# Kernel tuning notes

Measured on AMD Instinct MI355X. Metric: run time of the kernel, lower is better.

The kernel has to match this reference:

```python
import jax, jax.numpy as jnp
import numpy as np

N = 4096        # number_of_users
IN = 1000       # in_size (items)
H1, H2 = 2048, 1024
EMB = 512
HEADS = 8
OUT = 1000


def setup_inputs() -> dict:
    key = jax.random.key(0)
    ks = iter(jax.random.split(key, 32))
    def lin(i, o):
        return jax.random.normal(next(ks), (i, o), jnp.float32) * (1.0 / np.sqrt(i))
    inp = {"batch": jax.random.normal(next(ks), (N, IN), jnp.float32)}
    for p in ("q", "k", "v"):
        inp[p + "_w1"] = lin(IN, H1); inp[p + "_b1"] = jnp.zeros((H1,), jnp.float32)
        inp[p + "_w2"] = lin(H1, H2); inp[p + "_b2"] = jnp.zeros((H2,), jnp.float32)
        inp[p + "_w3"] = lin(H2, EMB); inp[p + "_b3"] = jnp.zeros((EMB,), jnp.float32)
    inp["wo_w"] = lin(EMB, OUT)
    inp["wo_b"] = jnp.zeros((OUT,), jnp.float32)
    return inp


def _mlp(x, w1, b1, w2, b2, w3, b3):
    h = jax.nn.relu(x @ w1 + b1)
    h = jax.nn.relu(h @ w2 + b2)
    return h @ w3 + b3


def _split_heads(x):
    # [N, EMB] -> [HEADS, N, depth]
    return x.reshape(N, HEADS, EMB // HEADS).transpose(1, 0, 2)


def reference(batch,
              q_w1, q_b1, q_w2, q_b2, q_w3, q_b3,
              k_w1, k_b1, k_w2, k_b2, k_w3, k_b3,
              v_w1, v_b1, v_w2, v_b2, v_w3, v_b3,
              wo_w, wo_b):
    q = _mlp(batch, q_w1, q_b1, q_w2, q_b2, q_w3, q_b3)
    k = _mlp(batch, k_w1, k_b1, k_w2, k_b2, k_w3, k_b3)
    v = _mlp(batch, v_w1, v_b1, v_w2, v_b2, v_w3, v_b3)
    qh = jax.nn.relu(_split_heads(q))
    kh = jax.nn.relu(_split_heads(k))
    vh = _split_heads(v)
    depth = EMB // HEADS
    # ReLU-normalized attention (no softmax): scores / row-sum
    scores = jnp.einsum('hnd,hmd->hnm', qh, kh) / jnp.sqrt(jnp.float32(depth))
    denom = jnp.sum(scores, axis=-1, keepdims=True) + 1e-8
    weights = scores / denom
    att = jnp.einsum('hnm,hmd->hnd', weights, vh)   # [H, N, depth]
    att = att.transpose(1, 0, 2).reshape(N, EMB)
    return att @ wo_w + wo_b
```

## Files before the change

kernel.cpp:

```cpp
#include <hip/hip_runtime.h>
#include <hip/hip_bf16.h>


typedef __attribute__((ext_vector_type(4))) float f32x4;
typedef __attribute__((ext_vector_type(4))) float float4v;
typedef __attribute__((ext_vector_type(8))) short bf16x8;

static constexpr size_t OFF_XB   = 0;
static constexpr size_t OFF_WT1  = OFF_XB   + 8388608;
static constexpr size_t OFF_WT2  = OFF_WT1  + 12582912;
static constexpr size_t OFF_WT3  = OFF_WT2  + 12582912;
static constexpr size_t OFF_MWT  = OFF_WT3  + 3145728;
static constexpr size_t OFF_B1C  = OFF_MWT  + 1048576;
static constexpr size_t OFF_H1   = OFF_B1C  + 24576;
static constexpr size_t OFF_H2   = OFF_H1   + 50331648;
static constexpr size_t OFF_QKV  = OFF_H2   + 25165824;
static constexpr size_t OFF_MP   = OFF_QKV  + 12582912;
static constexpr size_t OFF_MF   = OFF_MP   + 4259840;
static constexpr size_t OFF_QT   = OFF_MF   + 133120;

__device__ __forceinline__ void gload16(const __hip_bfloat16* g, __hip_bfloat16* l) {
  __builtin_amdgcn_global_load_lds(
      (const __attribute__((address_space(1))) void*)g,
      (__attribute__((address_space(3))) void*)l, 16, 0, 0);
}

__device__ __forceinline__ void xcd_map(int gx, int gy, int cm, int cn,
                                        int& zz, int& mt, int& nt) {
  const int gid = (blockIdx.z * gy + blockIdx.y) * gx + blockIdx.x;
  const int xcd = gid & 7;
  const int slot = gid >> 3;
  const int per = cm * cn;
  zz = slot / per;
  const int rem = slot % per;
  const int nxr = gx / cn;
  const int xr = xcd % nxr, yr = xcd / nxr;
  mt = yr * cm + rem % cm;
  nt = xr * cn + rem / cm;
}

__global__ __launch_bounds__(256) void prep(
    const float* __restrict__ w1a, const float* __restrict__ w1b, const float* __restrict__ w1c,
    const float* __restrict__ w2a, const float* __restrict__ w2b, const float* __restrict__ w2c,
    const float* __restrict__ w3a, const float* __restrict__ w3b, const float* __restrict__ w3c,
    const float* __restrict__ batch,
    __hip_bfloat16* __restrict__ WT1, __hip_bfloat16* __restrict__ WT2,
    __hip_bfloat16* __restrict__ WT3, __hip_bfloat16* __restrict__ XB) {
  const int b = blockIdx.x, t = threadIdx.x;
  if (b >= 3456) {
    int idx = (b - 3456) * 256 + t;
    int row = idx >> 8, c4 = (idx & 255) * 4;
    __hip_bfloat16 o[4];
    if (c4 < 1000) {
      float4v v = *reinterpret_cast<const float4v*>(&batch[(size_t)row * 1000 + c4]);
#pragma unroll
      for (int j = 0; j < 4; ++j) o[j] = __float2bfloat16(v[j]);
    } else {
#pragma unroll
      for (int j = 0; j < 4; ++j) o[j] = __float2bfloat16(0.f);
    }
    *reinterpret_cast<ushort4*>(&XB[(size_t)row * 1024 + c4]) =
        *reinterpret_cast<const ushort4*>(o);
    return;
  }
  __shared__ float tl[64][65];
  const float* in; __hip_bfloat16* out; int K, N, Kpad, kb, nb;
  if (b < 1536) {
    int mat = b / 512, r = b % 512;
    const float* s[3] = {w1a, w1b, w1c};
    in = s[mat]; out = WT1 + (size_t)mat * 2048 * 1024;
    K = 1000; N = 2048; Kpad = 1024; kb = r & 15; nb = r >> 4;
  } else if (b < 3072) {
    int r = b - 1536; int mat = r / 512; r %= 512;
    const float* s[3] = {w2a, w2b, w2c};
    in = s[mat]; out = WT2 + (size_t)mat * 1024 * 2048;
    K = 2048; N = 1024; Kpad = 2048; kb = r & 31; nb = r >> 5;
  } else {
    int r = b - 3072; int mat = r / 128; r %= 128;
    const float* s[3] = {w3a, w3b, w3c};
    in = s[mat]; out = WT3 + (size_t)mat * 512 * 1024;
    K = 1024; N = 512; Kpad = 1024; kb = r & 15; nb = r >> 4;
  }
  const int kb64 = kb * 64, nb64 = nb * 64;
  const int trow = t >> 4, tc4 = (t & 15) * 4;
#pragma unroll
  for (int it = 0; it < 4; ++it) {
    const int kl = it * 16 + trow;
    const int k = kb64 + kl;
    float4v v = {0.f, 0.f, 0.f, 0.f};
    if (k < K) v = *reinterpret_cast<const float4v*>(&in[(size_t)k * N + nb64 + tc4]);
    tl[kl][tc4 + 0] = v[0]; tl[kl][tc4 + 1] = v[1];
    tl[kl][tc4 + 2] = v[2]; tl[kl][tc4 + 3] = v[3];
  }
  __syncthreads();
  const int ln = t >> 2, ks = (t & 3) * 16;
  short ob[16];
#pragma unroll
  for (int u = 0; u < 16; ++u) {
    __hip_bfloat16 bb = __float2bfloat16(tl[ks + u][ln]);
    ob[u] = *(const short*)&bb;
  }
  __hip_bfloat16* dst = out + (size_t)(nb64 + ln) * Kpad + kb64 + ks;
  *reinterpret_cast<bf16x8*>(dst) = *reinterpret_cast<const bf16x8*>(&ob[0]);
  *reinterpret_cast<bf16x8*>(dst + 8) = *reinterpret_cast<const bf16x8*>(&ob[8]);
}

template <int NJ, int MINW>
__global__ __launch_bounds__(256, MINW) void gemm_fast(
    const __hip_bfloat16* __restrict__ A, int lda, size_t Az,
    const __hip_bfloat16* __restrict__ B, int ldb, size_t Bz,
    const float* __restrict__ bias0, const float* __restrict__ bias1,
    const float* __restrict__ bias2,
    void* __restrict__ Cout, int ldc, size_t Cz,
    int nlimit, int NT, int epi, int cm, int cn) {
  __shared__ __hip_bfloat16 smA[2][4096];
  __shared__ __hip_bfloat16 smB[2][NJ * 1024];
  const int t = threadIdx.x;
  int zz, mt, nt;
  xcd_map(gridDim.x, gridDim.y, cm, cn, zz, mt, nt);
  const int m0 = mt * 128, n0 = nt * (NJ * 32);
  A += (size_t)zz * Az;
  B += (size_t)zz * Bz;

  const int w = t >> 6, l = t & 63;
  const int wm = (w >> 1) * 64, wn = (w & 1) * (NJ * 16);
  const int fr = l & 15, fq = l >> 4;

  const int r0 = t >> 2;
  const int cg = (t & 3) ^ ((t >> 3) & 3);
  const __hip_bfloat16* gA0 = A + (size_t)(m0 + r0) * lda + cg * 8;
  const __hip_bfloat16* gA1 = gA0 + (size_t)64 * lda;
  const __hip_bfloat16* gB0 = B + (size_t)(n0 + r0) * ldb + cg * 8;
  const __hip_bfloat16* gB1 = gB0 + (size_t)64 * ldb;

  const int soff = (fq ^ ((fr >> 1) & 3)) * 8;
  int offA[4], offB[NJ];
#pragma unroll
  for (int i = 0; i < 4; ++i) offA[i] = (wm + i * 16 + fr) * 32 + soff;
#pragma unroll
  for (int j = 0; j < NJ; ++j) offB[j] = (wn + j * 16 + fr) * 32 + soff;

  f32x4 acc[4][NJ] = {};

  gload16(gA0, &smA[0][w * 512]);
  gload16(gA1, &smA[0][w * 512 + 2048]);
  gload16(gB0, &smB[0][w * 512]);
  if (NJ == 4) gload16(gB1, &smB[0][w * 512 + 2048]);

  for (int T = 0; T < NT; ++T) {
    const int cur = T & 1, nxt = cur ^ 1;
    __syncthreads();
    if (T + 1 < NT) {
      const size_t ko = (size_t)(T + 1) * 32;
      gload16(gA0 + ko, &smA[nxt][w * 512]);
      gload16(gA1 + ko, &smA[nxt][w * 512 + 2048]);
      gload16(gB0 + ko, &smB[nxt][w * 512]);
      if (NJ == 4) gload16(gB1 + ko, &smB[nxt][w * 512 + 2048]);
    }
    bf16x8 af[4], bf[NJ];
#pragma unroll
    for (int i = 0; i < 4; ++i)
      af[i] = *reinterpret_cast<const bf16x8*>(&smA[cur][offA[i]]);
#pragma unroll
    for (int j = 0; j < NJ; ++j)
      bf[j] = *reinterpret_cast<const bf16x8*>(&smB[cur][offB[j]]);
#pragma unroll
    for (int i = 0; i < 4; ++i)
#pragma unroll
      for (int j = 0; j < NJ; ++j)
        acc[i][j] = __builtin_amdgcn_mfma_f32_16x16x32_bf16(af[i], bf[j], acc[i][j], 0, 0, 0);
  }

  const float* bz = (zz == 0) ? bias0 : ((zz == 1) ? bias1 : bias2);
  const bool dorelu = (epi == 1) || (epi == 4) || (epi == 3 && zz < 2);
  float bv[NJ];
#pragma unroll
  for (int j = 0; j < NJ; ++j) {
    const int col = n0 + wn + j * 16 + fr;
    if (epi == 4) {
      const float* bsel = (col < 2048) ? bias0 : ((col < 4096) ? bias1 : bias2);
      bv[j] = bsel[col & 2047];
    } else if (epi == 2) {
      bv[j] = (col < nlimit) ? bias0[col] : 0.f;
    } else {
      bv[j] = bz[col];
    }
  }
#pragma unroll
  for (int i = 0; i < 4; ++i) {
#pragma unroll
    for (int j = 0; j < NJ; ++j) {
      const int col = n0 + wn + j * 16 + fr;
#pragma unroll
      for (int rr = 0; rr < 4; ++rr) {
        const int row = m0 + wm + i * 16 + fq * 4 + rr;
        float v = acc[i][j][rr] + bv[j];
        if (dorelu) v = fmaxf(v, 0.f);
        if (epi == 2) {
          if (col < nlimit)
            ((float*)Cout)[(size_t)row * ldc + col] = v;
        } else {
          ((__hip_bfloat16*)Cout + (size_t)zz * Cz)[(size_t)row * ldc + col] =
              __float2bfloat16(v);
        }
      }
    }
  }
}

__global__ __launch_bounds__(256) void kv_outer(const __hip_bfloat16* __restrict__ QKV, int ld,
                                                float* __restrict__ part) {
  __shared__ __hip_bfloat16 kt[128][64];
  __shared__ __hip_bfloat16 vt[128][64];
  const int t = threadIdx.x;
  const int n0 = blockIdx.x * 128;
  const int h = blockIdx.y;
#pragma unroll
  for (int it = 0; it < 4; ++it) {
    int r = it * 32 + (t >> 3);
    int c = (t & 7) * 8;
    const __hip_bfloat16* kr = &QKV[(size_t)(n0 + r) * ld + 512 + h * 64 + c];
    const __hip_bfloat16* vr = &QKV[(size_t)(n0 + r) * ld + 1024 + h * 64 + c];
    *reinterpret_cast<bf16x8*>(&kt[r][c]) = *reinterpret_cast<const bf16x8*>(kr);
    *reinterpret_cast<bf16x8*>(&vt[r][c]) = *reinterpret_cast<const bf16x8*>(vr);
  }
  __syncthreads();
  const int i = t >> 2, j0 = (t & 3) << 4;
  float acc[16] = {};
  float ks = 0.f;
  for (int r = 0; r < 128; ++r) {
    float kv = __bfloat162float(kt[r][i]);
    ks += kv;
    bf16x8 va = *reinterpret_cast<const bf16x8*>(&vt[r][j0]);
    bf16x8 vb = *reinterpret_cast<const bf16x8*>(&vt[r][j0 + 8]);
#pragma unroll
    for (int jj = 0; jj < 8; ++jj) {
      ushort ua = (ushort)((const short*)&va)[jj];
      ushort ub = (ushort)((const short*)&vb)[jj];
      acc[jj]     += kv * __bfloat162float(*(const __hip_bfloat16*)&ua);
      acc[8 + jj] += kv * __bfloat162float(*(const __hip_bfloat16*)&ub);
    }
  }
  float* dst = part + ((size_t)blockIdx.x * 8 + h) * 4160;
#pragma unroll
  for (int jj = 0; jj < 16; ++jj) dst[i * 64 + j0 + jj] = acc[jj];
  if ((t & 3) == 0) dst[4096 + i] = ks;
}

__global__ void reduce_m(const float* __restrict__ part, float* __restrict__ Mfin) {
  int h = blockIdx.x, t = threadIdx.x;
  for (int idx = t; idx < 4160; idx += 256) {
    float s = 0.f;
    for (int c = 0; c < 32; ++c) s += part[((size_t)c * 8 + h) * 4160 + idx];
    Mfin[(size_t)h * 4160 + idx] = s;
  }
}

__global__ __launch_bounds__(256) void mwq(const float* __restrict__ Mfin,
                                           const float* __restrict__ wo,
                                           __hip_bfloat16* __restrict__ MWT,
                                           const __hip_bfloat16* __restrict__ QKV,
                                           __hip_bfloat16* __restrict__ QT) {
  const int t = threadIdx.x;
  if (blockIdx.x < 32) {
    __shared__ float Ml[64][64];
    const int h = blockIdx.x >> 2;
    const int j = (blockIdx.x & 3) * 256 + t;
    const float* M = Mfin + (size_t)h * 4160;
    for (int e = t; e < 4096; e += 256)
      Ml[e >> 6][e & 63] = M[e];
    __syncthreads();
    float wcol[64];
    const bool valid = (j < 1000);
#pragma unroll
    for (int d = 0; d < 64; ++d)
      wcol[d] = valid ? wo[(size_t)(h * 64 + d) * 1000 + j] : 0.f;
    short ob[64];
#pragma unroll
    for (int i = 0; i < 64; ++i) {
      float a = 0.f;
#pragma unroll
      for (int d = 0; d < 64; ++d) a += Ml[i][d] * wcol[d];
      __hip_bfloat16 bb = __float2bfloat16(a);
      ob[i] = *(const short*)&bb;
    }
    __hip_bfloat16* dst = MWT + (size_t)j * 512 + h * 64;
#pragma unroll
    for (int v = 0; v < 8; ++v)
      *reinterpret_cast<bf16x8*>(dst + v * 8) = *reinterpret_cast<const bf16x8*>(&ob[v * 8]);
  } else {
    const int bid = blockIdx.x - 32;
    const int r = bid * 4 + (t >> 6);
    const int c = (t & 63) * 8;
    const int h = (t & 63) >> 3;
    bf16x8 qv = *reinterpret_cast<const bf16x8*>(&QKV[(size_t)r * 1536 + c]);
    float qf[8];
#pragma unroll
    for (int j = 0; j < 8; ++j) {
      ushort u = (ushort)((const short*)&qv)[j];
      qf[j] = __bfloat162float(*(const __hip_bfloat16*)&u);
    }
    const float* ks = Mfin + (size_t)h * 4160 + 4096 + (c & 63);
    float s = 0.f;
#pragma unroll
    for (int j = 0; j < 8; ++j) s += qf[j] * ks[j];
    s += __shfl_xor(s, 1, 8);
    s += __shfl_xor(s, 2, 8);
    s += __shfl_xor(s, 4, 8);
    const float inv = 0.125f / (s * 0.125f + 1e-8f);
    bf16x8 o;
#pragma unroll
    for (int j = 0; j < 8; ++j) {
      __hip_bfloat16 bb = __float2bfloat16(qf[j] * inv);
      ((short*)&o)[j] = *(const short*)&bb;
    }
    *reinterpret_cast<bf16x8*>(&QT[(size_t)r * 512 + c]) = o;
  }
}

extern "C" void kernel_launch(void* const* d_in, const int* in_sizes, int n_in,
                              void* d_out, int out_size, void* d_ws, size_t ws_size,
                              hipStream_t stream) {
  const float* batch = (const float*)d_in[0];
  const float* w1[3] = {(const float*)d_in[1],  (const float*)d_in[7],  (const float*)d_in[13]};
  const float* b1[3] = {(const float*)d_in[2],  (const float*)d_in[8],  (const float*)d_in[14]};
  const float* w2[3] = {(const float*)d_in[3],  (const float*)d_in[9],  (const float*)d_in[15]};
  const float* b2[3] = {(const float*)d_in[4],  (const float*)d_in[10], (const float*)d_in[16]};
  const float* w3[3] = {(const float*)d_in[5],  (const float*)d_in[11], (const float*)d_in[17]};
  const float* b3[3] = {(const float*)d_in[6],  (const float*)d_in[12], (const float*)d_in[18]};
  const float* wow   = (const float*)d_in[19];
  const float* wob   = (const float*)d_in[20];

  char* ws = (char*)d_ws;
  __hip_bfloat16* XB  = (__hip_bfloat16*)(ws + OFF_XB);
  __hip_bfloat16* WT1 = (__hip_bfloat16*)(ws + OFF_WT1);
  __hip_bfloat16* WT2 = (__hip_bfloat16*)(ws + OFF_WT2);
  __hip_bfloat16* WT3 = (__hip_bfloat16*)(ws + OFF_WT3);
  __hip_bfloat16* MWT = (__hip_bfloat16*)(ws + OFF_MWT);
  __hip_bfloat16* H1  = (__hip_bfloat16*)(ws + OFF_H1);
  __hip_bfloat16* H2  = (__hip_bfloat16*)(ws + OFF_H2);
  __hip_bfloat16* QKV = (__hip_bfloat16*)(ws + OFF_QKV);
  float*          MP  = (float*)(ws + OFF_MP);
  float*          MF  = (float*)(ws + OFF_MF);
  __hip_bfloat16* QT  = (__hip_bfloat16*)(ws + OFF_QT);
  float*          OUT = (float*)d_out;

  prep<<<7552, 256, 0, stream>>>(w1[0], w1[1], w1[2], w2[0], w2[1], w2[2],
                                 w3[0], w3[1], w3[2], batch, WT1, WT2, WT3, XB);

  gemm_fast<4, 4><<<dim3(48, 32, 1), 256, 0, stream>>>(
      XB, 1024, 0, WT1, 1024, 0, b1[0], b1[1], b1[2], H1, 6144, 0,
      6144, 32, 4, 16, 12);
  gemm_fast<4, 4><<<dim3(8, 32, 3), 256, 0, stream>>>(
      H1, 6144, 2048, WT2, 2048, (size_t)1024 * 2048,
      b2[0], b2[1], b2[2], H2, 3072, 1024, 1024, 64, 1, 8, 4);
  gemm_fast<2, 4><<<dim3(8, 32, 3), 256, 0, stream>>>(
      H2, 3072, 1024, WT3, 1024, (size_t)512 * 1024,
      b3[0], b3[1], b3[2], QKV, 1536, 512, 512, 32, 3, 8, 4);

  kv_outer<<<dim3(32, 8), 256, 0, stream>>>(QKV, 1536, MP);
  reduce_m<<<8, 256, 0, stream>>>(MP, MF);
  mwq<<<1056, 256, 0, stream>>>(MF, wow, MWT, QKV, QT);

  gemm_fast<2, 4><<<dim3(16, 32, 1), 256, 0, stream>>>(
      QT, 512, 0, MWT, 512, 0, wob, wob, wob, OUT, 1000, 0,
      1000, 16, 2, 16, 4);

  (void)in_sizes; (void)n_in; (void)out_size; (void)ws_size;
}
```

Baseline: 285.9 us.

## Triple-buffer GEMM LDS pipeline with explicit vmcnt waits; parallelize reduce_m

```diff
diff --git a/kernel.cpp b/kernel.cpp
--- a/kernel.cpp
+++ b/kernel.cpp
@@ -105,16 +105,16 @@
   *reinterpret_cast<bf16x8*>(dst + 8) = *reinterpret_cast<const bf16x8*>(&ob[8]);
 }
 
-template <int NJ, int MINW>
-__global__ __launch_bounds__(256, MINW) void gemm_fast(
+template <int NJ>
+__global__ __launch_bounds__(256, 3) void gemm_fast(
     const __hip_bfloat16* __restrict__ A, int lda, size_t Az,
     const __hip_bfloat16* __restrict__ B, int ldb, size_t Bz,
     const float* __restrict__ bias0, const float* __restrict__ bias1,
     const float* __restrict__ bias2,
     void* __restrict__ Cout, int ldc, size_t Cz,
     int nlimit, int NT, int epi, int cm, int cn) {
-  __shared__ __hip_bfloat16 smA[2][4096];
-  __shared__ __hip_bfloat16 smB[2][NJ * 1024];
+  __shared__ __hip_bfloat16 smA[3][4096];
+  __shared__ __hip_bfloat16 smB[3][NJ * 1024];
   const int t = threadIdx.x;
   int zz, mt, nt;
   xcd_map(gridDim.x, gridDim.y, cm, cn, zz, mt, nt);
@@ -142,21 +142,27 @@
 
   f32x4 acc[4][NJ] = {};
 
-  gload16(gA0, &smA[0][w * 512]);
-  gload16(gA1, &smA[0][w * 512 + 2048]);
-  gload16(gB0, &smB[0][w * 512]);
-  if (NJ == 4) gload16(gB1, &smB[0][w * 512 + 2048]);
-
+#define STG(BUF, KT) do {                                                      \
+    const size_t ko_ = (size_t)(KT) * 32;                                      \
+    gload16(gA0 + ko_, &smA[BUF][w * 512]);                                    \
+    gload16(gA1 + ko_, &smA[BUF][w * 512 + 2048]);                             \
+    gload16(gB0 + ko_, &smB[BUF][w * 512]);                                    \
+    if (NJ == 4) gload16(gB1 + ko_, &smB[BUF][w * 512 + 2048]);                \
+  } while (0)
+
+  STG(0, 0);
+  STG(1, 1);
+
+  int cur = 0;
   for (int T = 0; T < NT; ++T) {
-    const int cur = T & 1, nxt = cur ^ 1;
-    __syncthreads();
-    if (T + 1 < NT) {
-      const size_t ko = (size_t)(T + 1) * 32;
-      gload16(gA0 + ko, &smA[nxt][w * 512]);
-      gload16(gA1 + ko, &smA[nxt][w * 512 + 2048]);
-      gload16(gB0 + ko, &smB[nxt][w * 512]);
-      if (NJ == 4) gload16(gB1 + ko, &smB[nxt][w * 512 + 2048]);
-    }
+    if (T == NT - 1)
+      asm volatile("s_waitcnt vmcnt(0)" ::: "memory");
+    else if (NJ == 4)
+      asm volatile("s_waitcnt vmcnt(4)" ::: "memory");
+    else
+      asm volatile("s_waitcnt vmcnt(3)" ::: "memory");
+    __builtin_amdgcn_s_barrier();
+    __builtin_amdgcn_sched_barrier(0);
     bf16x8 af[4], bf[NJ];
 #pragma unroll
     for (int i = 0; i < 4; ++i)
@@ -164,12 +170,18 @@
 #pragma unroll
     for (int j = 0; j < NJ; ++j)
       bf[j] = *reinterpret_cast<const bf16x8*>(&smB[cur][offB[j]]);
+    if (T + 2 < NT) {
+      const int nb_ = (cur + 2 >= 3) ? cur - 1 : cur + 2;
+      STG(nb_, T + 2);
+    }
 #pragma unroll
     for (int i = 0; i < 4; ++i)
 #pragma unroll
       for (int j = 0; j < NJ; ++j)
         acc[i][j] = __builtin_amdgcn_mfma_f32_16x16x32_bf16(af[i], bf[j], acc[i][j], 0, 0, 0);
-  }
+    cur = (cur + 1 >= 3) ? 0 : cur + 1;
+  }
+#undef STG
 
   const float* bz = (zz == 0) ? bias0 : ((zz == 1) ? bias1 : bias2);
   const bool dorelu = (epi == 1) || (epi == 4) || (epi == 3 && zz < 2);
@@ -247,13 +259,15 @@
   if ((t & 3) == 0) dst[4096 + i] = ks;
 }
 
-__global__ void reduce_m(const float* __restrict__ part, float* __restrict__ Mfin) {
-  int h = blockIdx.x, t = threadIdx.x;
-  for (int idx = t; idx < 4160; idx += 256) {
-    float s = 0.f;
-    for (int c = 0; c < 32; ++c) s += part[((size_t)c * 8 + h) * 4160 + idx];
-    Mfin[(size_t)h * 4160 + idx] = s;
-  }
+__global__ __launch_bounds__(256) void reduce_m(const float* __restrict__ part,
+                                                float* __restrict__ Mfin) {
+  const int g = blockIdx.x * 256 + threadIdx.x;
+  if (g >= 8 * 4160) return;
+  const int h = g / 4160, idx = g % 4160;
+  float s = 0.f;
+#pragma unroll 4
+  for (int c = 0; c < 32; ++c) s += part[((size_t)c * 8 + h) * 4160 + idx];
+  Mfin[(size_t)h * 4160 + idx] = s;
 }
 
 __global__ __launch_bounds__(256) void mwq(const float* __restrict__ Mfin,
@@ -348,21 +362,21 @@
   prep<<<7552, 256, 0, stream>>>(w1[0], w1[1], w1[2], w2[0], w2[1], w2[2],
                                  w3[0], w3[1], w3[2], batch, WT1, WT2, WT3, XB);
 
-  gemm_fast<4, 4><<<dim3(48, 32, 1), 256, 0, stream>>>(
+  gemm_fast<4><<<dim3(48, 32, 1), 256, 0, stream>>>(
       XB, 1024, 0, WT1, 1024, 0, b1[0], b1[1], b1[2], H1, 6144, 0,
       6144, 32, 4, 16, 12);
-  gemm_fast<4, 4><<<dim3(8, 32, 3), 256, 0, stream>>>(
+  gemm_fast<4><<<dim3(8, 32, 3), 256, 0, stream>>>(
       H1, 6144, 2048, WT2, 2048, (size_t)1024 * 2048,
       b2[0], b2[1], b2[2], H2, 3072, 1024, 1024, 64, 1, 8, 4);
-  gemm_fast<2, 4><<<dim3(8, 32, 3), 256, 0, stream>>>(
+  gemm_fast<2><<<dim3(8, 32, 3), 256, 0, stream>>>(
       H2, 3072, 1024, WT3, 1024, (size_t)512 * 1024,
       b3[0], b3[1], b3[2], QKV, 1536, 512, 512, 32, 3, 8, 4);
 
   kv_outer<<<dim3(32, 8), 256, 0, stream>>>(QKV, 1536, MP);
-  reduce_m<<<8, 256, 0, stream>>>(MP, MF);
+  reduce_m<<<130, 256, 0, stream>>>(MP, MF);
   mwq<<<1056, 256, 0, stream>>>(MF, wow, MWT, QKV, QT);
 
-  gemm_fast<2, 4><<<dim3(16, 32, 1), 256, 0, stream>>>(
+  gemm_fast<2><<<dim3(16, 32, 1), 256, 0, stream>>>(
       QT, 512, 0, MWT, 512, 0, wob, wob, wob, OUT, 1000, 0,
       1000, 16, 2, 16, 4);
 
```

Result: faster. 237.9 us (median of 2 runs) (-16.8%).
